# Performance work log

Measured on AMD Instinct MI355X. Metric: run time of the kernel, lower is better.

## Reference

```python
import jax, jax.numpy as jnp
import numpy as np

D_MODEL = 1024
NUM_HEADS = 16
D_K = D_MODEL // NUM_HEADS


def setup_inputs() -> dict:
    key = jax.random.key(0)
    ks = jax.random.split(key, 9)
    s = 1.0 / np.sqrt(D_MODEL)
    x = jax.random.normal(ks[0], (2, 2048, D_MODEL), dtype=jnp.float32)
    Wq = jax.random.uniform(ks[1], (D_MODEL, D_MODEL), jnp.float32, -s, s)
    bq = jax.random.uniform(ks[2], (D_MODEL,), jnp.float32, -s, s)
    Wk = jax.random.uniform(ks[3], (D_MODEL, D_MODEL), jnp.float32, -s, s)
    bk = jax.random.uniform(ks[4], (D_MODEL,), jnp.float32, -s, s)
    Wv = jax.random.uniform(ks[5], (D_MODEL, D_MODEL), jnp.float32, -s, s)
    bv = jax.random.uniform(ks[6], (D_MODEL,), jnp.float32, -s, s)
    Wo = jax.random.uniform(ks[7], (D_MODEL, D_MODEL), jnp.float32, -s, s)
    bo = jax.random.uniform(ks[8], (D_MODEL,), jnp.float32, -s, s)
    return {"x": x, "Wq": Wq, "bq": bq, "Wk": Wk, "bk": bk,
            "Wv": Wv, "bv": bv, "Wo": Wo, "bo": bo}


def reference(x, Wq, bq, Wk, bk, Wv, bv, Wo, bo):
    B, S, _ = x.shape
    # torch Linear: y = x @ W.T + b
    def proj(W, b):
        h = x @ W.T + b                       # [B,S,D]
        return h.reshape(B, S, NUM_HEADS, D_K).transpose(0, 2, 1, 3)  # [B,H,S,Dk]
    Q = proj(Wq, bq)
    K = proj(Wk, bk)
    V = proj(Wv, bv)
    scale = 1.0 / np.sqrt(D_K)
    scores = jnp.einsum('bhqd,bhkd->bhqk', Q, K) * scale   # [B,H,S,S]
    causal = jnp.triu(jnp.ones((S, S), dtype=bool), k=1)   # True above diag
    scores = jnp.where(causal, -jnp.inf, scores)
    probs = jax.nn.softmax(scores, axis=-1)
    out = jnp.einsum('bhqk,bhkd->bhqd', probs, V)          # [B,H,S,Dk]
    out = out.transpose(0, 2, 1, 3).reshape(B, S, NUM_HEADS * D_K)
    return out @ Wo.T + bo
```

## Files before the change

kernel.cpp:

```cpp
#include <hip/hip_runtime.h>

typedef unsigned short u16;
typedef __attribute__((ext_vector_type(8))) short short8;
typedef __attribute__((ext_vector_type(4))) float floatx4;

__device__ __forceinline__ u16 f2bf(float x){
  union { float f; unsigned u; } v; v.f = x;
  unsigned r = v.u + 0x7fffu + ((v.u >> 16) & 1u);
  return (u16)(r >> 16);
}

__device__ __forceinline__ unsigned cvt_pk_bf16(float lo, float hi){
  unsigned r;
  asm("v_cvt_pk_bf16_f32 %0, %1, %2" : "=v"(r) : "v"(lo), "v"(hi));
  return r;
}

__device__ __forceinline__ float exp2_raw(float x){
  float r;
  asm("v_exp_f32 %0, %1" : "=v"(r) : "v"(x));
  return r;
}

__device__ __forceinline__ void gld16(const u16* g, u16* l){
  __builtin_amdgcn_global_load_lds(
      (const __attribute__((address_space(1))) void*)g,
      (__attribute__((address_space(3))) void*)l, 16, 0, 0);
}

#define WAIT_BAR_V4() asm volatile("s_waitcnt vmcnt(4) lgkmcnt(0)\ns_barrier" ::: "memory")
#define WAIT_BAR_V3() asm volatile("s_waitcnt vmcnt(3) lgkmcnt(0)\ns_barrier" ::: "memory")
#define WAIT_BAR_V0() asm volatile("s_waitcnt vmcnt(0) lgkmcnt(0)\ns_barrier" ::: "memory")

__global__ void k_cvt_all(const float* __restrict__ x,
                          const float* __restrict__ wq, const float* __restrict__ wk,
                          const float* __restrict__ wv, const float* __restrict__ wo,
                          u16* __restrict__ xb, u16* __restrict__ wqb, u16* __restrict__ wkb,
                          u16* __restrict__ wvb, u16* __restrict__ wob){
  const int i = blockIdx.x * 256 + threadIdx.x;
  const float* s; u16* d; int off;
  if (i < 1048576) { s = x; d = xb; off = i; }
  else {
    const int j = i - 1048576;
    const int wsel = j >> 18;
    off = j & 262143;
    s = (wsel==0) ? wq : (wsel==1) ? wk : (wsel==2) ? wv : wo;
    d = (wsel==0) ? wqb : (wsel==1) ? wkb : (wsel==2) ? wvb : wob;
  }
  const float4 f = ((const float4*)s)[off];
  unsigned lo = (unsigned)f2bf(f.x) | ((unsigned)f2bf(f.y) << 16);
  unsigned hi = (unsigned)f2bf(f.z) | ((unsigned)f2bf(f.w) << 16);
  ((uint2*)d)[off] = make_uint2(lo, hi);
}

__global__ __launch_bounds__(256) void k_gemm_qkv(
    const u16* __restrict__ A,
    const u16* __restrict__ Wq, const u16* __restrict__ Wk, const u16* __restrict__ Wv,
    const float* __restrict__ bq, const float* __restrict__ bk, const float* __restrict__ bv,
    u16* __restrict__ Qo, u16* __restrict__ Ko, u16* __restrict__ Vo)
{
  const int bid = (int)blockIdx.x;
  const int xcd = bid & 7;
  const int i5  = bid >> 3;
  const int xb_ = ((xcd >> 2) << 2) + (i5 & 3);
  const int rest = i5 >> 2;
  const int yb_ = ((xcd & 3) << 3) + (rest & 7);
  const int mode = rest >> 3;

  const u16* W      = (mode==1) ? Wk : (mode==2) ? Wv : Wq;
  const float* bias = (mode==1) ? bk : (mode==2) ? bv : bq;

  __shared__ u16 lA[3][4096];
  __shared__ u16 lB[3][4096];

  const int tid  = threadIdx.x;
  const int row0 = yb_ * 128;
  const int col0 = xb_ * 128;

  const int srow = tid >> 2;
  const int sgp  = tid & 3;
  const int sgl  = sgp ^ ((srow >> 1) & 3);
  const u16* ga0 = A + (row0 + srow)      * 1024 + sgl * 8;
  const u16* ga1 = A + (row0 + srow + 64) * 1024 + sgl * 8;
  const u16* gb0 = W + (col0 + srow)      * 1024 + sgl * 8;
  const u16* gb1 = W + (col0 + srow + 64) * 1024 + sgl * 8;

  const int l  = tid & 63, w = tid >> 6;
  const int wr = w >> 1,  wc = w & 1;
  const int lr = l & 15,  grp = l >> 4;
  const int sw = (lr >> 1) & 3;
  int aoff[4], boff[4];
#pragma unroll
  for (int m = 0; m < 4; ++m) aoff[m] = (wr*64 + m*16 + lr)*32 + ((grp ^ sw) * 8);
#pragma unroll
  for (int n = 0; n < 4; ++n) boff[n] = (wc*64 + n*16 + lr)*32 + ((grp ^ sw) * 8);

  floatx4 acc[4][4];
#pragma unroll
  for (int m = 0; m < 4; ++m)
#pragma unroll
    for (int n = 0; n < 4; ++n) acc[m][n] = (floatx4){0.f, 0.f, 0.f, 0.f};

#define STAGE(buf, kt_) do { \
    const int k0_ = (kt_) * 32; \
    gld16(ga0 + k0_, &lA[(buf)][tid*8]); \
    gld16(ga1 + k0_, &lA[(buf)][2048 + tid*8]); \
    gld16(gb0 + k0_, &lB[(buf)][tid*8]); \
    gld16(gb1 + k0_, &lB[(buf)][2048 + tid*8]); \
  } while (0)

  STAGE(0, 0);
  STAGE(1, 1);
  asm volatile("s_waitcnt vmcnt(4)\ns_barrier" ::: "memory");

  for (int kt0 = 0; kt0 < 32; kt0 += 3) {
#pragma unroll
    for (int i = 0; i < 3; ++i) {
      const int kt = kt0 + i;
      if (kt >= 32) break;
      const bool st2 = (kt + 2 < 32);
      if (st2) STAGE((i + 2) % 3, kt + 2);
      short8 af[4], bf[4];
#pragma unroll
      for (int m = 0; m < 4; ++m) af[m] = *(const short8*)&lA[i][aoff[m]];
#pragma unroll
      for (int n = 0; n < 4; ++n) bf[n] = *(const short8*)&lB[i][boff[n]];
#pragma unroll
      for (int m = 0; m < 4; ++m)
#pragma unroll
        for (int n = 0; n < 4; ++n)
          acc[m][n] = __builtin_amdgcn_mfma_f32_16x16x32_bf16(af[m], bf[n], acc[m][n], 0, 0, 0);
      if (st2) WAIT_BAR_V4(); else WAIT_BAR_V0();
    }
  }
#undef STAGE

  const float sc = (mode == 0) ? 0.18033688011112042f : 1.0f;
  u16* dst = (mode == 0) ? Qo : (mode == 1) ? Ko : Vo;
#pragma unroll
  for (int n = 0; n < 4; ++n) {
    const int cg = col0 + wc*64 + n*16 + lr;
    const float bb = bias[cg];
    const int h = cg >> 6, d = cg & 63;
#pragma unroll
    for (int m = 0; m < 4; ++m) {
#pragma unroll
      for (int j = 0; j < 4; ++j) {
        const int rg = row0 + wr*64 + m*16 + grp*4 + j;
        const int b = rg >> 11, s5 = rg & 2047;
        const float val = (acc[m][n][j] + bb) * sc;
        int idx;
        if (mode == 2) idx = ((b*16 + h)*64 + d)*2048 + s5;
        else           idx = ((b*16 + h)*2048 + s5)*64 + d;
        dst[idx] = f2bf(val);
      }
    }
  }
}

__global__ __launch_bounds__(256) void k_gemm_o(
    const u16* __restrict__ A, const u16* __restrict__ W,
    const float* __restrict__ bias, float* __restrict__ Fo)
{
  const int bid = (int)blockIdx.x;
  const int xcd = bid & 7;
  const int i5  = bid >> 3;
  const int xb_ = ((xcd >> 2) << 2) + (i5 & 3);
  const int yb_ = ((xcd & 3) << 4) + (i5 >> 2);

  __shared__ u16 lA[3][2048];
  __shared__ u16 lB[3][4096];

  const int tid  = threadIdx.x;
  const int row0 = yb_ * 64;
  const int col0 = xb_ * 128;

  const int srow = tid >> 2;
  const int sgp  = tid & 3;
  const int sgl  = sgp ^ ((srow >> 1) & 3);
  const u16* ga0 = A + (row0 + srow)      * 1024 + sgl * 8;
  const u16* gb0 = W + (col0 + srow)      * 1024 + sgl * 8;
  const u16* gb1 = W + (col0 + srow + 64) * 1024 + sgl * 8;

  const int l  = tid & 63, w = tid >> 6;
  const int wr = w >> 1,  wc = w & 1;
  const int lr = l & 15,  grp = l >> 4;
  const int sw = (lr >> 1) & 3;
  int aoff[2], boff[4];
#pragma unroll
  for (int m = 0; m < 2; ++m) aoff[m] = (wr*32 + m*16 + lr)*32 + ((grp ^ sw) * 8);
#pragma unroll
  for (int n = 0; n < 4; ++n) boff[n] = (wc*64 + n*16 + lr)*32 + ((grp ^ sw) * 8);

  floatx4 acc[2][4];
#pragma unroll
  for (int m = 0; m < 2; ++m)
#pragma unroll
    for (int n = 0; n < 4; ++n) acc[m][n] = (floatx4){0.f, 0.f, 0.f, 0.f};

#define STAGE(buf, kt_) do { \
    const int k0_ = (kt_) * 32; \
    gld16(ga0 + k0_, &lA[(buf)][tid*8]); \
    gld16(gb0 + k0_, &lB[(buf)][tid*8]); \
    gld16(gb1 + k0_, &lB[(buf)][2048 + tid*8]); \
  } while (0)

  STAGE(0, 0);
  STAGE(1, 1);
  asm volatile("s_waitcnt vmcnt(3)\ns_barrier" ::: "memory");

  for (int kt0 = 0; kt0 < 32; kt0 += 3) {
#pragma unroll
    for (int i = 0; i < 3; ++i) {
      const int kt = kt0 + i;
      if (kt >= 32) break;
      const bool st2 = (kt + 2 < 32);
      if (st2) STAGE((i + 2) % 3, kt + 2);
      short8 af[2], bf[4];
#pragma unroll
      for (int m = 0; m < 2; ++m) af[m] = *(const short8*)&lA[i][aoff[m]];
#pragma unroll
      for (int n = 0; n < 4; ++n) bf[n] = *(const short8*)&lB[i][boff[n]];
#pragma unroll
      for (int m = 0; m < 2; ++m)
#pragma unroll
        for (int n = 0; n < 4; ++n)
          acc[m][n] = __builtin_amdgcn_mfma_f32_16x16x32_bf16(af[m], bf[n], acc[m][n], 0, 0, 0);
      if (st2) WAIT_BAR_V3(); else WAIT_BAR_V0();
    }
  }
#undef STAGE

#pragma unroll
  for (int n = 0; n < 4; ++n) {
    const int cg = col0 + wc*64 + n*16 + lr;
    const float bb = bias[cg];
#pragma unroll
    for (int m = 0; m < 2; ++m) {
      const int rg = row0 + wr*32 + m*16 + grp*4;
#pragma unroll
      for (int j = 0; j < 4; ++j)
        Fo[(rg + j) * 1024 + cg] = acc[m][n][j] + bb;
    }
  }
}

__global__ __launch_bounds__(256, 4) void k_attn(
    const u16* __restrict__ Q, const u16* __restrict__ K,
    const u16* __restrict__ V, u16* __restrict__ O)
{
  __shared__ u16 lK[2][4096];
  __shared__ u16 lV[2][4096];
  __shared__ u16 lP[4][1024];

  const int tid = threadIdx.x;
  const int bid = (int)blockIdx.x;
  const int xcd = bid & 7, r = bid >> 3;
  const int k_ = r & 31, j_ = r >> 5;
  const int bh = xcd * 4 + j_;
  const int qt = (j_ & 1) ? k_ : (31 - k_);

  const int l = tid & 63, w = tid >> 6;
  const int lr = l & 15, grp = l >> 4;
  const int qw0 = qt * 64 + w * 16;
  const int nkt = qt + 1;

  const u16* Qh = Q + (size_t)bh * 2048 * 64;
  const u16* Kh = K + (size_t)bh * 2048 * 64;
  const u16* Vh = V + (size_t)bh * 64 * 2048;

  const int srow = tid >> 3, sgp = tid & 7;
  const int sgl = sgp ^ (srow & 7);
  u16* lPw = &lP[w][0];
  const int swz = lr & 7;
  const int b = bh >> 4, h = bh & 15;

#define STAGEKV(buf, kt_) do { \
    gld16(Kh + ((kt_)*64 + srow     )*64 + sgl*8, &lK[(buf)][tid*8]); \
    gld16(Kh + ((kt_)*64 + srow + 32)*64 + sgl*8, &lK[(buf)][2048 + tid*8]); \
    gld16(Vh + (srow     )*2048 + (kt_)*64 + sgl*8, &lV[(buf)][tid*8]); \
    gld16(Vh + (srow + 32)*2048 + (kt_)*64 + sgl*8, &lV[(buf)][2048 + tid*8]); \
  } while (0)

  short8 qf[2];
#pragma unroll
  for (int kk = 0; kk < 2; ++kk)
    qf[kk] = *(const short8*)(Qh + (qw0 + lr)*64 + kk*32 + grp*8);

  floatx4 accO[4];
  float mrow = -1e30f, lrow = 0.f;
#pragma unroll
  for (int dn = 0; dn < 4; ++dn) accO[dn] = (floatx4){0.f, 0.f, 0.f, 0.f};

  STAGEKV(0, 0);
  __syncthreads();

  for (int kt0 = 0; kt0 < nkt; kt0 += 2) {
#pragma unroll
    for (int i = 0; i < 2; ++i) {
      const int kt = kt0 + i;
      if (kt >= nkt) break;
      if (kt + 1 < nkt) STAGEKV(i ^ 1, kt + 1);
      const int kb = kt * 64;

      floatx4 st[4];
#pragma unroll
      for (int n = 0; n < 4; ++n) st[n] = (floatx4){0.f, 0.f, 0.f, 0.f};
#pragma unroll
      for (int n = 0; n < 4; ++n) {
        const int key = n*16 + lr;
#pragma unroll
        for (int kk = 0; kk < 2; ++kk) {
          const int gp = (kk*4 + grp) ^ (key & 7);
          short8 kf = *(const short8*)&lK[i][key*64 + gp*8];
          st[n] = __builtin_amdgcn_mfma_f32_16x16x32_bf16(kf, qf[kk], st[n], 0, 0, 0);
        }
      }

      const int lim = qw0 + lr - kb;
      if (63 > lim) {
#pragma unroll
        for (int n = 0; n < 4; ++n)
#pragma unroll
          for (int jj = 0; jj < 4; ++jj)
            if (n*16 + grp*4 + jj > lim) st[n][jj] = -1e30f;
      }

      float mt = st[0][0];
#pragma unroll
      for (int n = 0; n < 4; ++n)
#pragma unroll
        for (int jj = 0; jj < 4; ++jj) mt = fmaxf(mt, st[n][jj]);
      if (!__all(mt <= mrow)) {
        float mg = fmaxf(mt, __shfl_xor(mt, 16));
        mg = fmaxf(mg, __shfl_xor(mg, 32));
        const float mn = fmaxf(mrow, mg);
        const float alpha = exp2_raw(mrow - mn);
        mrow = mn;
        lrow *= alpha;
#pragma unroll
        for (int dn = 0; dn < 4; ++dn) accO[dn] *= alpha;
      }
      float ps = 0.f;
#pragma unroll
      for (int n = 0; n < 4; ++n)
#pragma unroll
        for (int jj = 0; jj < 4; ++jj) {
          const float p = exp2_raw(st[n][jj] - mrow);
          st[n][jj] = p;
          ps += p;
        }
      lrow += ps;

#pragma unroll
      for (int n = 0; n < 4; ++n)
#pragma unroll
        for (int p2 = 0; p2 < 2; ++p2) {
          const unsigned pk = cvt_pk_bf16(st[n][2*p2], st[n][2*p2+1]);
          const int pg = (2*n + (grp >> 1)) ^ swz;
          ((unsigned*)lPw)[lr*32 + pg*4 + (grp & 1)*2 + p2] = pk;
        }

      asm volatile("s_waitcnt lgkmcnt(0)" ::: "memory");

      short8 pa[2];
#pragma unroll
      for (int kk = 0; kk < 2; ++kk)
        pa[kk] = *(const short8*)&lPw[lr*64 + (((kk*4 + grp) ^ swz) * 8)];

#pragma unroll
      for (int dn = 0; dn < 4; ++dn) {
        const int d = dn*16 + lr;
#pragma unroll
        for (int kk = 0; kk < 2; ++kk) {
          const int gp = (kk*4 + grp) ^ (d & 7);
          short8 vf = *(const short8*)&lV[i][d*64 + gp*8];
          accO[dn] = __builtin_amdgcn_mfma_f32_16x16x32_bf16(vf, pa[kk], accO[dn], 0, 0, 0);
        }
      }
      __syncthreads();
    }
  }

  float lt = lrow + __shfl_xor(lrow, 16);
  lt += __shfl_xor(lt, 32);
  const float inv = 1.0f / lt;
  const int token = b*2048 + qw0 + lr;
#pragma unroll
  for (int dn = 0; dn < 4; ++dn)
#pragma unroll
    for (int p2 = 0; p2 < 2; ++p2) {
      const unsigned pk = cvt_pk_bf16(accO[dn][2*p2] * inv, accO[dn][2*p2+1] * inv);
      *(unsigned*)&O[token*1024 + h*64 + dn*16 + grp*4 + 2*p2] = pk;
    }
#undef STAGEKV
}

extern "C" void kernel_launch(void* const* d_in, const int* in_sizes, int n_in,
                              void* d_out, int out_size, void* d_ws, size_t ws_size,
                              hipStream_t stream) {
  const float* x  = (const float*)d_in[0];
  const float* Wq = (const float*)d_in[1];
  const float* bq = (const float*)d_in[2];
  const float* Wk = (const float*)d_in[3];
  const float* bk = (const float*)d_in[4];
  const float* Wv = (const float*)d_in[5];
  const float* bv = (const float*)d_in[6];
  const float* Wo = (const float*)d_in[7];
  const float* bo = (const float*)d_in[8];
  float* out = (float*)d_out;

  char* ws = (char*)d_ws;
  u16* xb  = (u16*)(ws + 0);
  u16* wqb = (u16*)(ws + 8388608);
  u16* wkb = (u16*)(ws + 10485760);
  u16* wvb = (u16*)(ws + 12582912);
  u16* wob = (u16*)(ws + 14680064);
  u16* Qb  = (u16*)(ws + 16777216);
  u16* Kb  = (u16*)(ws + 25165824);
  u16* Vb  = (u16*)(ws + 33554432);
  u16* Ab  = (u16*)(ws + 41943040);

  k_cvt_all<<<dim3(8192), 256, 0, stream>>>(x, Wq, Wk, Wv, Wo, xb, wqb, wkb, wvb, wob);

  k_gemm_qkv<<<dim3(768), 256, 0, stream>>>(xb, wqb, wkb, wvb, bq, bk, bv, Qb, Kb, Vb);

  k_attn<<<dim3(1024), 256, 0, stream>>>(Qb, Kb, Vb, Ab);

  k_gemm_o<<<dim3(512), 256, 0, stream>>>(Ab, wob, bo, out);
}
```

Measured before the change: 110.4 us.

## Shrink QKV GEMM and attention blocks to two waves with larger per-wave tiles

The QKV projection GEMM now runs two waves per block instead of four. Each wave computes a 64x128 output tile with 32 accumulators, so every LDS fragment feeds more MFMAs, and each thread issues eight global-to-LDS loads per stage. The attention kernel also moves to two-wave blocks covering 32 query rows, which doubles the grid to 2048 blocks for finer causal load balancing. The cost is that K/V tiles are fetched twice as often per query row, and the GEMM uses more registers per wave.

```diff
diff --git a/kernel.cpp b/kernel.cpp
--- a/kernel.cpp
+++ b/kernel.cpp
@@ -28,7 +28,7 @@
       (__attribute__((address_space(3))) void*)l, 16, 0, 0);
 }
 
-#define WAIT_BAR_V4() asm volatile("s_waitcnt vmcnt(4) lgkmcnt(0)\ns_barrier" ::: "memory")
+#define WAIT_BAR_V8() asm volatile("s_waitcnt vmcnt(8) lgkmcnt(0)\ns_barrier" ::: "memory")
 #define WAIT_BAR_V3() asm volatile("s_waitcnt vmcnt(3) lgkmcnt(0)\ns_barrier" ::: "memory")
 #define WAIT_BAR_V0() asm volatile("s_waitcnt vmcnt(0) lgkmcnt(0)\ns_barrier" ::: "memory")
 
@@ -53,7 +53,7 @@
   ((uint2*)d)[off] = make_uint2(lo, hi);
 }
 
-__global__ __launch_bounds__(256) void k_gemm_qkv(
+__global__ __launch_bounds__(128, 2) void k_gemm_qkv(
     const u16* __restrict__ A,
     const u16* __restrict__ Wq, const u16* __restrict__ Wk, const u16* __restrict__ Wv,
     const float* __restrict__ bq, const float* __restrict__ bk, const float* __restrict__ bv,
@@ -80,38 +80,39 @@
   const int srow = tid >> 2;
   const int sgp  = tid & 3;
   const int sgl  = sgp ^ ((srow >> 1) & 3);
-  const u16* ga0 = A + (row0 + srow)      * 1024 + sgl * 8;
-  const u16* ga1 = A + (row0 + srow + 64) * 1024 + sgl * 8;
-  const u16* gb0 = W + (col0 + srow)      * 1024 + sgl * 8;
-  const u16* gb1 = W + (col0 + srow + 64) * 1024 + sgl * 8;
+  const u16* ga = A + (row0 + srow) * 1024 + sgl * 8;
+  const u16* gb = W + (col0 + srow) * 1024 + sgl * 8;
 
   const int l  = tid & 63, w = tid >> 6;
-  const int wr = w >> 1,  wc = w & 1;
   const int lr = l & 15,  grp = l >> 4;
   const int sw = (lr >> 1) & 3;
-  int aoff[4], boff[4];
-#pragma unroll
-  for (int m = 0; m < 4; ++m) aoff[m] = (wr*64 + m*16 + lr)*32 + ((grp ^ sw) * 8);
-#pragma unroll
-  for (int n = 0; n < 4; ++n) boff[n] = (wc*64 + n*16 + lr)*32 + ((grp ^ sw) * 8);
-
-  floatx4 acc[4][4];
+  int aoff[4], boff[8];
+#pragma unroll
+  for (int m = 0; m < 4; ++m) aoff[m] = (w*64 + m*16 + lr)*32 + ((grp ^ sw) * 8);
+#pragma unroll
+  for (int n = 0; n < 8; ++n) boff[n] = (n*16 + lr)*32 + ((grp ^ sw) * 8);
+
+  floatx4 acc[4][8];
 #pragma unroll
   for (int m = 0; m < 4; ++m)
 #pragma unroll
-    for (int n = 0; n < 4; ++n) acc[m][n] = (floatx4){0.f, 0.f, 0.f, 0.f};
+    for (int n = 0; n < 8; ++n) acc[m][n] = (floatx4){0.f, 0.f, 0.f, 0.f};
 
 #define STAGE(buf, kt_) do { \
     const int k0_ = (kt_) * 32; \
-    gld16(ga0 + k0_, &lA[(buf)][tid*8]); \
-    gld16(ga1 + k0_, &lA[(buf)][2048 + tid*8]); \
-    gld16(gb0 + k0_, &lB[(buf)][tid*8]); \
-    gld16(gb1 + k0_, &lB[(buf)][2048 + tid*8]); \
+    gld16(ga + k0_,                &lA[(buf)][tid*8]); \
+    gld16(ga + k0_ + 32*1024,      &lA[(buf)][1024 + tid*8]); \
+    gld16(ga + k0_ + 64*1024,      &lA[(buf)][2048 + tid*8]); \
+    gld16(ga + k0_ + 96*1024,      &lA[(buf)][3072 + tid*8]); \
+    gld16(gb + k0_,                &lB[(buf)][tid*8]); \
+    gld16(gb + k0_ + 32*1024,      &lB[(buf)][1024 + tid*8]); \
+    gld16(gb + k0_ + 64*1024,      &lB[(buf)][2048 + tid*8]); \
+    gld16(gb + k0_ + 96*1024,      &lB[(buf)][3072 + tid*8]); \
   } while (0)
 
   STAGE(0, 0);
   STAGE(1, 1);
-  asm volatile("s_waitcnt vmcnt(4)\ns_barrier" ::: "memory");
+  asm volatile("s_waitcnt vmcnt(8)\ns_barrier" ::: "memory");
 
   for (int kt0 = 0; kt0 < 32; kt0 += 3) {
 #pragma unroll
@@ -120,17 +121,17 @@
       if (kt >= 32) break;
       const bool st2 = (kt + 2 < 32);
       if (st2) STAGE((i + 2) % 3, kt + 2);
-      short8 af[4], bf[4];
+      short8 af[4], bf[8];
 #pragma unroll
       for (int m = 0; m < 4; ++m) af[m] = *(const short8*)&lA[i][aoff[m]];
 #pragma unroll
-      for (int n = 0; n < 4; ++n) bf[n] = *(const short8*)&lB[i][boff[n]];
+      for (int n = 0; n < 8; ++n) bf[n] = *(const short8*)&lB[i][boff[n]];
 #pragma unroll
       for (int m = 0; m < 4; ++m)
 #pragma unroll
-        for (int n = 0; n < 4; ++n)
+        for (int n = 0; n < 8; ++n)
           acc[m][n] = __builtin_amdgcn_mfma_f32_16x16x32_bf16(af[m], bf[n], acc[m][n], 0, 0, 0);
-      if (st2) WAIT_BAR_V4(); else WAIT_BAR_V0();
+      if (st2) WAIT_BAR_V8(); else WAIT_BAR_V0();
     }
   }
 #undef STAGE
@@ -138,15 +139,15 @@
   const float sc = (mode == 0) ? 0.18033688011112042f : 1.0f;
   u16* dst = (mode == 0) ? Qo : (mode == 1) ? Ko : Vo;
 #pragma unroll
-  for (int n = 0; n < 4; ++n) {
-    const int cg = col0 + wc*64 + n*16 + lr;
+  for (int n = 0; n < 8; ++n) {
+    const int cg = col0 + n*16 + lr;
     const float bb = bias[cg];
     const int h = cg >> 6, d = cg & 63;
 #pragma unroll
     for (int m = 0; m < 4; ++m) {
 #pragma unroll
       for (int j = 0; j < 4; ++j) {
-        const int rg = row0 + wr*64 + m*16 + grp*4 + j;
+        const int rg = row0 + w*64 + m*16 + grp*4 + j;
         const int b = rg >> 11, s5 = rg & 2047;
         const float val = (acc[m][n][j] + bb) * sc;
         int idx;
@@ -245,25 +246,24 @@
   }
 }
 
-__global__ __launch_bounds__(256, 4) void k_attn(
+__global__ __launch_bounds__(128, 2) void k_attn(
     const u16* __restrict__ Q, const u16* __restrict__ K,
     const u16* __restrict__ V, u16* __restrict__ O)
 {
   __shared__ u16 lK[2][4096];
   __shared__ u16 lV[2][4096];
-  __shared__ u16 lP[4][1024];
+  __shared__ u16 lP[2][1024];
 
   const int tid = threadIdx.x;
   const int bid = (int)blockIdx.x;
-  const int xcd = bid & 7, r = bid >> 3;
-  const int k_ = r & 31, j_ = r >> 5;
-  const int bh = xcd * 4 + j_;
-  const int qt = (j_ & 1) ? k_ : (31 - k_);
+  const int xcd = bid & 7, lid = bid >> 3;
+  const int bh = xcd * 4 + (lid & 3);
+  const int t  = 63 - (lid >> 2);
 
   const int l = tid & 63, w = tid >> 6;
   const int lr = l & 15, grp = l >> 4;
-  const int qw0 = qt * 64 + w * 16;
-  const int nkt = qt + 1;
+  const int qw0 = t * 32 + w * 16;
+  const int nkt = (t >> 1) + 1;
 
   const u16* Qh = Q + (size_t)bh * 2048 * 64;
   const u16* Kh = K + (size_t)bh * 2048 * 64;
@@ -277,9 +277,13 @@
 
 #define STAGEKV(buf, kt_) do { \
     gld16(Kh + ((kt_)*64 + srow     )*64 + sgl*8, &lK[(buf)][tid*8]); \
+    gld16(Kh + ((kt_)*64 + srow + 16)*64 + sgl*8, &lK[(buf)][1024 + tid*8]); \
     gld16(Kh + ((kt_)*64 + srow + 32)*64 + sgl*8, &lK[(buf)][2048 + tid*8]); \
+    gld16(Kh + ((kt_)*64 + srow + 48)*64 + sgl*8, &lK[(buf)][3072 + tid*8]); \
     gld16(Vh + (srow     )*2048 + (kt_)*64 + sgl*8, &lV[(buf)][tid*8]); \
+    gld16(Vh + (srow + 16)*2048 + (kt_)*64 + sgl*8, &lV[(buf)][1024 + tid*8]); \
     gld16(Vh + (srow + 32)*2048 + (kt_)*64 + sgl*8, &lV[(buf)][2048 + tid*8]); \
+    gld16(Vh + (srow + 48)*2048 + (kt_)*64 + sgl*8, &lV[(buf)][3072 + tid*8]); \
   } while (0)
 
   short8 qf[2];
@@ -423,9 +427,9 @@
 
   k_cvt_all<<<dim3(8192), 256, 0, stream>>>(x, Wq, Wk, Wv, Wo, xb, wqb, wkb, wvb, wob);
 
-  k_gemm_qkv<<<dim3(768), 256, 0, stream>>>(xb, wqb, wkb, wvb, bq, bk, bv, Qb, Kb, Vb);
-
-  k_attn<<<dim3(1024), 256, 0, stream>>>(Qb, Kb, Vb, Ab);
+  k_gemm_qkv<<<dim3(768), 128, 0, stream>>>(xb, wqb, wkb, wvb, bq, bk, bv, Qb, Kb, Vb);
+
+  k_attn<<<dim3(2048), 128, 0, stream>>>(Qb, Kb, Vb, Ab);
 
   k_gemm_o<<<dim3(512), 256, 0, stream>>>(Ab, wob, bo, out);
 }
```

Measured after the change: 116.4 us. +5.5%, slower.

## Restructure attention into single-wave blocks with 32x32 MFMA and register P shuffles

Applied to the files above, without the earlier changes.

The attention kernel moves from 256-thread blocks over 64-query tiles to 64-thread single-wave blocks over 32-query tiles and 32-key tiles. It uses 32x32x16 bf16 MFMAs and passes the probability matrix between the QK and PV MFMAs through cross-half lane shuffles instead of an LDS round trip. Block barriers are replaced by explicit vmcnt waits. This is meant to remove LDS traffic and sync overhead and to balance the causal work across more blocks, but each block now does more K/V staging per query and may get lower occupancy from the launch bounds.

```diff
diff --git a/kernel.cpp b/kernel.cpp
--- a/kernel.cpp
+++ b/kernel.cpp
@@ -3,6 +3,7 @@
 typedef unsigned short u16;
 typedef __attribute__((ext_vector_type(8))) short short8;
 typedef __attribute__((ext_vector_type(4))) float floatx4;
+typedef __attribute__((ext_vector_type(16))) float floatx16;
 
 __device__ __forceinline__ u16 f2bf(float x){
   union { float f; unsigned u; } v; v.f = x;
@@ -245,155 +246,153 @@
   }
 }
 
-__global__ __launch_bounds__(256, 4) void k_attn(
+__global__ __launch_bounds__(64, 2) void k_attn(
     const u16* __restrict__ Q, const u16* __restrict__ K,
     const u16* __restrict__ V, u16* __restrict__ O)
 {
-  __shared__ u16 lK[2][4096];
-  __shared__ u16 lV[2][4096];
-  __shared__ u16 lP[4][1024];
+  __shared__ u16 lK[2][2048];
+  __shared__ u16 lV[2][2048];
 
   const int tid = threadIdx.x;
   const int bid = (int)blockIdx.x;
-  const int xcd = bid & 7, r = bid >> 3;
-  const int k_ = r & 31, j_ = r >> 5;
-  const int bh = xcd * 4 + j_;
-  const int qt = (j_ & 1) ? k_ : (31 - k_);
-
-  const int l = tid & 63, w = tid >> 6;
-  const int lr = l & 15, grp = l >> 4;
-  const int qw0 = qt * 64 + w * 16;
-  const int nkt = qt + 1;
+  const int xcd = bid & 7, lid = bid >> 3;
+  const int bh = xcd * 4 + (lid & 3);
+  const int t  = 63 - (lid >> 2);
+  const int nkt = t + 1;
+
+  const int l = tid;
+  const int q_lane = l & 31, h = l >> 5;
+  const int qw0 = t * 32;
+  const bool lo_half = (h == 0);
 
   const u16* Qh = Q + (size_t)bh * 2048 * 64;
   const u16* Kh = K + (size_t)bh * 2048 * 64;
   const u16* Vh = V + (size_t)bh * 64 * 2048;
 
-  const int srow = tid >> 3, sgp = tid & 7;
-  const int sgl = sgp ^ (srow & 7);
-  u16* lPw = &lP[w][0];
-  const int swz = lr & 7;
-  const int b = bh >> 4, h = bh & 15;
+  const int krow = tid >> 3;
+  const int ksg  = (tid & 7) ^ krow;
+  const int vrow = tid >> 2;
+  const int vsg  = (tid & 3) ^ (vrow & 3);
 
 #define STAGEKV(buf, kt_) do { \
-    gld16(Kh + ((kt_)*64 + srow     )*64 + sgl*8, &lK[(buf)][tid*8]); \
-    gld16(Kh + ((kt_)*64 + srow + 32)*64 + sgl*8, &lK[(buf)][2048 + tid*8]); \
-    gld16(Vh + (srow     )*2048 + (kt_)*64 + sgl*8, &lV[(buf)][tid*8]); \
-    gld16(Vh + (srow + 32)*2048 + (kt_)*64 + sgl*8, &lV[(buf)][2048 + tid*8]); \
+    const int kb_ = (kt_) * 32; \
+    gld16(Kh + (kb_ + 0*8 + krow)*64 + ksg*8, &lK[(buf)][0*512 + tid*8]); \
+    gld16(Kh + (kb_ + 1*8 + krow)*64 + ksg*8, &lK[(buf)][1*512 + tid*8]); \
+    gld16(Kh + (kb_ + 2*8 + krow)*64 + ksg*8, &lK[(buf)][2*512 + tid*8]); \
+    gld16(Kh + (kb_ + 3*8 + krow)*64 + ksg*8, &lK[(buf)][3*512 + tid*8]); \
+    gld16(Vh + (0*16 + vrow)*2048 + kb_ + vsg*8, &lV[(buf)][0*512 + tid*8]); \
+    gld16(Vh + (1*16 + vrow)*2048 + kb_ + vsg*8, &lV[(buf)][1*512 + tid*8]); \
+    gld16(Vh + (2*16 + vrow)*2048 + kb_ + vsg*8, &lV[(buf)][2*512 + tid*8]); \
+    gld16(Vh + (3*16 + vrow)*2048 + kb_ + vsg*8, &lV[(buf)][3*512 + tid*8]); \
   } while (0)
 
-  short8 qf[2];
-#pragma unroll
-  for (int kk = 0; kk < 2; ++kk)
-    qf[kk] = *(const short8*)(Qh + (qw0 + lr)*64 + kk*32 + grp*8);
-
-  floatx4 accO[4];
+  short8 qf[4];
+#pragma unroll
+  for (int i4 = 0; i4 < 4; ++i4)
+    qf[i4] = *(const short8*)(Qh + (qw0 + q_lane)*64 + (2*i4 + h)*8);
+
+  floatx16 accO[2];
+  accO[0] = (floatx16)(0.0f);
+  accO[1] = (floatx16)(0.0f);
   float mrow = -1e30f, lrow = 0.f;
-#pragma unroll
-  for (int dn = 0; dn < 4; ++dn) accO[dn] = (floatx4){0.f, 0.f, 0.f, 0.f};
+
+  const int ksw = q_lane & 7;
+  const int vsw = q_lane & 3;
+  const int hd = bh & 15, b = bh >> 4;
 
   STAGEKV(0, 0);
-  __syncthreads();
 
   for (int kt0 = 0; kt0 < nkt; kt0 += 2) {
 #pragma unroll
     for (int i = 0; i < 2; ++i) {
       const int kt = kt0 + i;
       if (kt >= nkt) break;
-      if (kt + 1 < nkt) STAGEKV(i ^ 1, kt + 1);
-      const int kb = kt * 64;
-
-      floatx4 st[4];
-#pragma unroll
-      for (int n = 0; n < 4; ++n) st[n] = (floatx4){0.f, 0.f, 0.f, 0.f};
-#pragma unroll
-      for (int n = 0; n < 4; ++n) {
-        const int key = n*16 + lr;
-#pragma unroll
-        for (int kk = 0; kk < 2; ++kk) {
-          const int gp = (kk*4 + grp) ^ (key & 7);
-          short8 kf = *(const short8*)&lK[i][key*64 + gp*8];
-          st[n] = __builtin_amdgcn_mfma_f32_16x16x32_bf16(kf, qf[kk], st[n], 0, 0, 0);
+      asm volatile("" ::: "memory");
+      if (kt + 1 < nkt) {
+        STAGEKV(i ^ 1, kt + 1);
+        asm volatile("s_waitcnt vmcnt(8)" ::: "memory");
+      } else {
+        asm volatile("s_waitcnt vmcnt(0)" ::: "memory");
+      }
+
+      floatx16 st = (floatx16)(0.0f);
+#pragma unroll
+      for (int i4 = 0; i4 < 4; ++i4) {
+        short8 kf = *(const short8*)&lK[i][q_lane*64 + (((2*i4 + h) ^ ksw) * 8)];
+        st = __builtin_amdgcn_mfma_f32_32x32x16_bf16(kf, qf[i4], st, 0, 0, 0);
+      }
+
+      if (kt == nkt - 1) {
+#pragma unroll
+        for (int r = 0; r < 16; ++r) {
+          const int koff = (r & 3) + 8*(r >> 2) + 4*h;
+          if (koff > q_lane) st[r] = -1e30f;
         }
       }
 
-      const int lim = qw0 + lr - kb;
-      if (63 > lim) {
-#pragma unroll
-        for (int n = 0; n < 4; ++n)
-#pragma unroll
-          for (int jj = 0; jj < 4; ++jj)
-            if (n*16 + grp*4 + jj > lim) st[n][jj] = -1e30f;
-      }
-
-      float mt = st[0][0];
-#pragma unroll
-      for (int n = 0; n < 4; ++n)
-#pragma unroll
-        for (int jj = 0; jj < 4; ++jj) mt = fmaxf(mt, st[n][jj]);
+      float mt = st[0];
+#pragma unroll
+      for (int r = 1; r < 16; ++r) mt = fmaxf(mt, st[r]);
       if (!__all(mt <= mrow)) {
-        float mg = fmaxf(mt, __shfl_xor(mt, 16));
-        mg = fmaxf(mg, __shfl_xor(mg, 32));
+        float mg = fmaxf(mt, __shfl_xor(mt, 32));
         const float mn = fmaxf(mrow, mg);
         const float alpha = exp2_raw(mrow - mn);
         mrow = mn;
         lrow *= alpha;
 #pragma unroll
-        for (int dn = 0; dn < 4; ++dn) accO[dn] *= alpha;
+        for (int r = 0; r < 16; ++r) { accO[0][r] *= alpha; accO[1][r] *= alpha; }
       }
       float ps = 0.f;
 #pragma unroll
-      for (int n = 0; n < 4; ++n)
-#pragma unroll
-        for (int jj = 0; jj < 4; ++jj) {
-          const float p = exp2_raw(st[n][jj] - mrow);
-          st[n][jj] = p;
-          ps += p;
+      for (int r = 0; r < 16; ++r) {
+        const float p = exp2_raw(st[r] - mrow);
+        st[r] = p;
+        ps += p;
+      }
+      lrow += ps;
+
+      unsigned P2[8];
+#pragma unroll
+      for (int r2 = 0; r2 < 8; ++r2) P2[r2] = cvt_pk_bf16(st[2*r2], st[2*r2+1]);
+      short8 pb[2];
+#pragma unroll
+      for (int ks = 0; ks < 2; ++ks) {
+        const unsigned A0 = P2[4*ks],     A1 = P2[4*ks + 1];
+        const unsigned B0 = P2[4*ks + 2], B1 = P2[4*ks + 3];
+        const unsigned sA0 = __shfl_xor(A0, 32), sA1 = __shfl_xor(A1, 32);
+        const unsigned sB0 = __shfl_xor(B0, 32), sB1 = __shfl_xor(B1, 32);
+        union { unsigned u[4]; short8 s; } pu;
+        pu.u[0] = lo_half ? A0 : sB0;
+        pu.u[1] = lo_half ? A1 : sB1;
+        pu.u[2] = lo_half ? sA0 : B0;
+        pu.u[3] = lo_half ? sA1 : B1;
+        pb[ks] = pu.s;
+      }
+
+#pragma unroll
+      for (int dn = 0; dn < 2; ++dn) {
+        const int vr = dn*32 + q_lane;
+#pragma unroll
+        for (int ks = 0; ks < 2; ++ks) {
+          short8 vf = *(const short8*)&lV[i][vr*32 + (((2*ks + h) ^ vsw) * 8)];
+          accO[dn] = __builtin_amdgcn_mfma_f32_32x32x16_bf16(vf, pb[ks], accO[dn], 0, 0, 0);
         }
-      lrow += ps;
-
-#pragma unroll
-      for (int n = 0; n < 4; ++n)
-#pragma unroll
-        for (int p2 = 0; p2 < 2; ++p2) {
-          const unsigned pk = cvt_pk_bf16(st[n][2*p2], st[n][2*p2+1]);
-          const int pg = (2*n + (grp >> 1)) ^ swz;
-          ((unsigned*)lPw)[lr*32 + pg*4 + (grp & 1)*2 + p2] = pk;
-        }
-
-      asm volatile("s_waitcnt lgkmcnt(0)" ::: "memory");
-
-      short8 pa[2];
-#pragma unroll
-      for (int kk = 0; kk < 2; ++kk)
-        pa[kk] = *(const short8*)&lPw[lr*64 + (((kk*4 + grp) ^ swz) * 8)];
-
-#pragma unroll
-      for (int dn = 0; dn < 4; ++dn) {
-        const int d = dn*16 + lr;
-#pragma unroll
-        for (int kk = 0; kk < 2; ++kk) {
-          const int gp = (kk*4 + grp) ^ (d & 7);
-          short8 vf = *(const short8*)&lV[i][d*64 + gp*8];
-          accO[dn] = __builtin_amdgcn_mfma_f32_16x16x32_bf16(vf, pa[kk], accO[dn], 0, 0, 0);
-        }
-      }
-      __syncthreads();
-    }
-  }
-
-  float lt = lrow + __shfl_xor(lrow, 16);
-  lt += __shfl_xor(lt, 32);
+      }
+    }
+  }
+#undef STAGEKV
+
+  float lt = lrow + __shfl_xor(lrow, 32);
   const float inv = 1.0f / lt;
-  const int token = b*2048 + qw0 + lr;
-#pragma unroll
-  for (int dn = 0; dn < 4; ++dn)
-#pragma unroll
-    for (int p2 = 0; p2 < 2; ++p2) {
-      const unsigned pk = cvt_pk_bf16(accO[dn][2*p2] * inv, accO[dn][2*p2+1] * inv);
-      *(unsigned*)&O[token*1024 + h*64 + dn*16 + grp*4 + 2*p2] = pk;
-    }
-#undef STAGEKV
+  const int token = b*2048 + qw0 + q_lane;
+#pragma unroll
+  for (int dn = 0; dn < 2; ++dn)
+#pragma unroll
+    for (int m = 0; m < 8; ++m) {
+      const int d = dn*32 + ((2*m) & 3) + 8*(m >> 1) + 4*h;
+      const unsigned pk = cvt_pk_bf16(accO[dn][2*m] * inv, accO[dn][2*m+1] * inv);
+      *(unsigned*)&O[token*1024 + hd*64 + d] = pk;
+    }
 }
 
 extern "C" void kernel_launch(void* const* d_in, const int* in_sizes, int n_in,
@@ -425,7 +424,7 @@
 
   k_gemm_qkv<<<dim3(768), 256, 0, stream>>>(xb, wqb, wkb, wvb, bq, bk, bv, Qb, Kb, Vb);
 
-  k_attn<<<dim3(1024), 256, 0, stream>>>(Qb, Kb, Vb, Ab);
+  k_attn<<<dim3(2048), 64, 0, stream>>>(Qb, Kb, Vb, Ab);
 
   k_gemm_o<<<dim3(512), 256, 0, stream>>>(Ab, wob, bo, out);
 }
```

New measurement: 130.5 us. 1.18x slower.

## Split KV range for long causal query tiles and merge partial outputs

Applied to the files above, without the earlier changes.

Query tiles in the upper half of the causal range (qt >= 16) now have their key range split across two blocks. Each half writes an unnormalized bf16 partial output plus its row max and sum. A new merge kernel rescales and combines the two partials into the attention output. This shortens the longest blocks to even out the causal workload, at the cost of a larger grid, an extra kernel launch, more global traffic, and bf16 rounding of the unnormalized partials.

```diff
diff --git a/kernel.cpp b/kernel.cpp
--- a/kernel.cpp
+++ b/kernel.cpp
@@ -8,6 +8,11 @@
   union { float f; unsigned u; } v; v.f = x;
   unsigned r = v.u + 0x7fffu + ((v.u >> 16) & 1u);
   return (u16)(r >> 16);
+}
+
+__device__ __forceinline__ float bf2f(u16 x){
+  union { unsigned u; float f; } v; v.u = ((unsigned)x) << 16;
+  return v.f;
 }
 
 __device__ __forceinline__ unsigned cvt_pk_bf16(float lo, float hi){
@@ -247,7 +252,8 @@
 
 __global__ __launch_bounds__(256, 4) void k_attn(
     const u16* __restrict__ Q, const u16* __restrict__ K,
-    const u16* __restrict__ V, u16* __restrict__ O)
+    const u16* __restrict__ V, u16* __restrict__ O,
+    u16* __restrict__ Opart, float* __restrict__ ml)
 {
   __shared__ u16 lK[2][4096];
   __shared__ u16 lV[2][4096];
@@ -255,15 +261,30 @@
 
   const int tid = threadIdx.x;
   const int bid = (int)blockIdx.x;
-  const int xcd = bid & 7, r = bid >> 3;
-  const int k_ = r & 31, j_ = r >> 5;
-  const int bh = xcd * 4 + j_;
-  const int qt = (j_ & 1) ? k_ : (31 - k_);
+  const int xcd = bid & 7, lid = bid >> 3;
+  const int s = lid >> 2, bhl = lid & 3;
+  const int bh = xcd * 4 + bhl;
+
+  int qt, beg, end, split = 0, qth = 0;
+  bool issplit;
+  if (s < 32) {
+    qt = 31 - (s >> 1);
+    split = s & 1;
+    const int h0 = (qt + 2) >> 1;
+    beg = split ? h0 : 0;
+    end = split ? (qt + 1) : h0;
+    issplit = true;
+    qth = qt - 16;
+  } else {
+    qt = 47 - s;
+    beg = 0;
+    end = qt + 1;
+    issplit = false;
+  }
 
   const int l = tid & 63, w = tid >> 6;
   const int lr = l & 15, grp = l >> 4;
   const int qw0 = qt * 64 + w * 16;
-  const int nkt = qt + 1;
 
   const u16* Qh = Q + (size_t)bh * 2048 * 64;
   const u16* Kh = K + (size_t)bh * 2048 * 64;
@@ -292,15 +313,17 @@
 #pragma unroll
   for (int dn = 0; dn < 4; ++dn) accO[dn] = (floatx4){0.f, 0.f, 0.f, 0.f};
 
-  STAGEKV(0, 0);
+  STAGEKV(0, beg);
   __syncthreads();
 
-  for (int kt0 = 0; kt0 < nkt; kt0 += 2) {
+  const int nloc = end - beg;
+  for (int p0 = 0; p0 < nloc; p0 += 2) {
 #pragma unroll
     for (int i = 0; i < 2; ++i) {
-      const int kt = kt0 + i;
-      if (kt >= nkt) break;
-      if (kt + 1 < nkt) STAGEKV(i ^ 1, kt + 1);
+      const int p = p0 + i;
+      if (p >= nloc) break;
+      const int kt = beg + p;
+      if (p + 1 < nloc) STAGEKV(i ^ 1, kt + 1);
       const int kb = kt * 64;
 
       floatx4 st[4];
@@ -346,9 +369,9 @@
       for (int n = 0; n < 4; ++n)
 #pragma unroll
         for (int jj = 0; jj < 4; ++jj) {
-          const float p = exp2_raw(st[n][jj] - mrow);
-          st[n][jj] = p;
-          ps += p;
+          const float p2v = exp2_raw(st[n][jj] - mrow);
+          st[n][jj] = p2v;
+          ps += p2v;
         }
       lrow += ps;
 
@@ -381,19 +404,65 @@
       __syncthreads();
     }
   }
+#undef STAGEKV
 
   float lt = lrow + __shfl_xor(lrow, 16);
   lt += __shfl_xor(lt, 32);
-  const float inv = 1.0f / lt;
-  const int token = b*2048 + qw0 + lr;
-#pragma unroll
-  for (int dn = 0; dn < 4; ++dn)
-#pragma unroll
-    for (int p2 = 0; p2 < 2; ++p2) {
-      const unsigned pk = cvt_pk_bf16(accO[dn][2*p2] * inv, accO[dn][2*p2+1] * inv);
-      *(unsigned*)&O[token*1024 + h*64 + dn*16 + grp*4 + 2*p2] = pk;
+  if (!issplit) {
+    const float inv = 1.0f / lt;
+    const int token = b*2048 + qw0 + lr;
+#pragma unroll
+    for (int dn = 0; dn < 4; ++dn)
+#pragma unroll
+      for (int p2 = 0; p2 < 2; ++p2) {
+        const unsigned pk = cvt_pk_bf16(accO[dn][2*p2] * inv, accO[dn][2*p2+1] * inv);
+        *(unsigned*)&O[token*1024 + h*64 + dn*16 + grp*4 + 2*p2] = pk;
+      }
+  } else {
+    const int q = w*16 + lr;
+    u16* Op = Opart + (size_t)((((bh*16 + qth)*2 + split)*64 + q) * 64);
+#pragma unroll
+    for (int dn = 0; dn < 4; ++dn)
+#pragma unroll
+      for (int p2 = 0; p2 < 2; ++p2) {
+        const unsigned pk = cvt_pk_bf16(accO[dn][2*p2], accO[dn][2*p2+1]);
+        *(unsigned*)&Op[dn*16 + grp*4 + 2*p2] = pk;
+      }
+    if (grp == 0) {
+      float* mlp = ml + (size_t)(((bh*16 + qth)*2 + split)*2) * 64;
+      mlp[q]      = mrow;
+      mlp[64 + q] = lt;
     }
-#undef STAGEKV
+  }
+}
+
+__global__ __launch_bounds__(256) void k_merge(
+    const u16* __restrict__ Opart, const float* __restrict__ ml,
+    u16* __restrict__ O)
+{
+  const int tile = (int)blockIdx.x;
+  const int bh = tile >> 4, qth = tile & 15;
+  const int qt = 16 + qth;
+  const int d = threadIdx.x & 63, qg = threadIdx.x >> 6;
+  const int b = bh >> 4, h = bh & 15;
+
+  const float* ml1 = ml + (size_t)((tile*2 + 0)*2) * 64;
+  const float* ml2 = ml + (size_t)((tile*2 + 1)*2) * 64;
+  const u16* O1 = Opart + (size_t)((tile*2 + 0)*64) * 64;
+  const u16* O2 = Opart + (size_t)((tile*2 + 1)*64) * 64;
+
+  for (int q0 = 0; q0 < 64; q0 += 4) {
+    const int q = q0 + qg;
+    const float m1 = ml1[q], l1 = ml1[64 + q];
+    const float m2 = ml2[q], l2 = ml2[64 + q];
+    const float m  = fmaxf(m1, m2);
+    const float a1 = exp2_raw(m1 - m), a2 = exp2_raw(m2 - m);
+    const float linv = 1.0f / (l1*a1 + l2*a2);
+    const float o1 = bf2f(O1[q*64 + d]);
+    const float o2 = bf2f(O2[q*64 + d]);
+    const int token = b*2048 + qt*64 + q;
+    O[token*1024 + h*64 + d] = f2bf((o1*a1 + o2*a2) * linv);
+  }
 }
 
 extern "C" void kernel_launch(void* const* d_in, const int* in_sizes, int n_in,
@@ -420,12 +489,16 @@
   u16* Kb  = (u16*)(ws + 25165824);
   u16* Vb  = (u16*)(ws + 33554432);
   u16* Ab  = (u16*)(ws + 41943040);
+  u16*   Opart = (u16*)(ws + 0);
+  float* mlbuf = (float*)(ws + 8388608);
 
   k_cvt_all<<<dim3(8192), 256, 0, stream>>>(x, Wq, Wk, Wv, Wo, xb, wqb, wkb, wvb, wob);
 
   k_gemm_qkv<<<dim3(768), 256, 0, stream>>>(xb, wqb, wkb, wvb, bq, bk, bv, Qb, Kb, Vb);
 
-  k_attn<<<dim3(1024), 256, 0, stream>>>(Qb, Kb, Vb, Ab);
+  k_attn<<<dim3(1536), 256, 0, stream>>>(Qb, Kb, Vb, Ab, Opart, mlbuf);
+
+  k_merge<<<dim3(512), 256, 0, stream>>>(Opart, mlbuf, Ab);
 
   k_gemm_o<<<dim3(512), 256, 0, stream>>>(Ab, wob, bo, out);
 }
```

After: 121.7 us. +10.3%, slower.
